# Kernel optimization log

Hardware: AMD Instinct MI355X
Metric: run time of the kernel (lower is better)

## Reference

```python
import jax, jax.numpy as jnp
import numpy as np

N_NODES = 50000
N_EDGES = 800000
IN_DIM = 128
HID = 32
HEADS = 4
OUT_DIM = 64
NEG_SLOPE = 0.2
EPS = 1e-16


def _gat_conv(x, src, dst, W, a_src, a_dst, b, heads, ch):
    """PyG GATConv (with self-loops already appended to src/dst), concat=True."""
    N = x.shape[0]
    h = (x @ W).reshape(N, heads, ch)                      # [N,H,C]
    alpha_s = jnp.einsum('nhc,hc->nh', h, a_src)           # [N,H]
    alpha_d = jnp.einsum('nhc,hc->nh', h, a_dst)           # [N,H]
    e = jax.nn.leaky_relu(alpha_s[src] + alpha_d[dst], NEG_SLOPE)  # [E,H]
    emax = jax.ops.segment_max(e, dst, num_segments=N)     # segment softmax over dst
    ex = jnp.exp(e - emax[dst])
    denom = jax.ops.segment_sum(ex, dst, num_segments=N)
    alpha = ex / (denom[dst] + EPS)                        # [E,H]
    out = jax.ops.segment_sum(h[src] * alpha[:, :, None], dst, num_segments=N)
    return out.reshape(N, heads * ch) + b


def setup_inputs() -> dict:
    key = jax.random.key(0)
    ks = jax.random.split(key, 16)
    x = jax.random.normal(ks[0], (N_NODES, IN_DIM), dtype=jnp.float32)
    edge_index = jax.random.randint(ks[1], (2, N_EDGES), 0, N_NODES, dtype=jnp.int64)

    def glorot(k, shape):
        fan = sum(shape[-2:]) if len(shape) > 1 else shape[-1]
        return jax.random.normal(k, shape, dtype=jnp.float32) * np.sqrt(2.0 / fan)

    # layer 0: IN_DIM -> HID x HEADS
    W0 = glorot(ks[2], (IN_DIM, HEADS * HID))
    as0 = glorot(ks[3], (HEADS, HID))
    ad0 = glorot(ks[4], (HEADS, HID))
    b0 = jnp.zeros((HEADS * HID,), jnp.float32)
    # layer 1: HID*HEADS -> HID x HEADS
    W1 = glorot(ks[5], (HEADS * HID, HEADS * HID))
    as1 = glorot(ks[6], (HEADS, HID))
    ad1 = glorot(ks[7], (HEADS, HID))
    b1 = jnp.zeros((HEADS * HID,), jnp.float32)
    # layer 2: HID*HEADS -> OUT_DIM, heads=1
    W2 = glorot(ks[8], (HEADS * HID, OUT_DIM))
    as2 = glorot(ks[9], (1, OUT_DIM))
    ad2 = glorot(ks[10], (1, OUT_DIM))
    b2 = jnp.zeros((OUT_DIM,), jnp.float32)
    return {"x": x, "edge_index": edge_index,
            "W0": W0, "as0": as0, "ad0": ad0, "b0": b0,
            "W1": W1, "as1": as1, "ad1": ad1, "b1": b1,
            "W2": W2, "as2": as2, "ad2": ad2, "b2": b2}


def reference(x, edge_index, W0, as0, ad0, b0, W1, as1, ad1, b1, W2, as2, ad2, b2):
    N = x.shape[0]
    # PyG GATConv default add_self_loops=True
    loops = jnp.arange(N, dtype=edge_index.dtype)
    src = jnp.concatenate([edge_index[0], loops])
    dst = jnp.concatenate([edge_index[1], loops])
    h = _gat_conv(x, src, dst, W0, as0, ad0, b0, HEADS, HID)
    h = _gat_conv(h, src, dst, W1, as1, ad1, b1, HEADS, HID)
    h = _gat_conv(h, src, dst, W2, as2, ad2, b2, 1, OUT_DIM)
    return h
```

## Files before the change

### kernel.cpp

```cpp
#include <hip/hip_runtime.h>
#include <hip/hip_fp16.h>
#include <cstdint>
#include <cstddef>

#define NEG_SLOPE 0.2f
#define EPS_F 1e-16f
#define NBLKB 64

static __device__ __forceinline__ float leaky(float x) { return x > 0.f ? x : NEG_SLOPE * x; }


__global__ __launch_bounds__(1024) void scan_k(const int* __restrict__ cnt, int* __restrict__ off, int N) {
    __shared__ int wsum[16];
    int tid = threadIdx.x;
    int lane = tid & 63, wid = tid >> 6;
    int running = 0;
    for (int base = 0; base < N; base += 1024) {
        int i = base + tid;
        int v = (i < N) ? cnt[i] : 0;
        int iv = v;
        #pragma unroll
        for (int d = 1; d < 64; d <<= 1) {
            int t = __shfl_up(iv, d);
            if (lane >= d) iv += t;
        }
        if (lane == 63) wsum[wid] = iv;
        __syncthreads();
        if (tid < 16) {
            int s = wsum[tid];
            #pragma unroll
            for (int d = 1; d < 16; d <<= 1) {
                int t = __shfl_up(s, d);
                if (tid >= d) s += t;
            }
            wsum[tid] = s;
        }
        __syncthreads();
        int add = wid ? wsum[wid - 1] : 0;
        if (i < N) off[i + 1] = running + add + iv;
        int ct = wsum[15];
        __syncthreads();
        running += ct;
    }
    if (tid == 0) off[0] = 0;
}


__global__ __launch_bounds__(256) void partB_k(const int* __restrict__ src, const int* __restrict__ dst,
                                               const int* __restrict__ starts, int* __restrict__ packed,
                                               int E, int nbuk) {
    __shared__ int lcnt[256];
    __shared__ int lbase[256];
    const int blk = blockIdx.x;
    for (int i = threadIdx.x; i < nbuk; i += 256) { lcnt[i] = 0; lbase[i] = starts[i * NBLKB + blk]; }
    __syncthreads();
    const int chunk = (E + NBLKB - 1) / NBLKB;
    const int base = blk * chunk, end = min(base + chunk, E);
    for (int i = base + (int)threadIdx.x; i < end; i += 256) {
        int d = dst[i], s = src[i];
        int b = d >> 8;
        int slot = atomicAdd(&lcnt[b], 1);
        packed[lbase[b] + slot] = s | ((d & 255) << 16);
    }
}

__global__ __launch_bounds__(256) void partC_k(const int* __restrict__ packed, const int* __restrict__ starts,
                                               int* __restrict__ off, int* __restrict__ esrc,
                                               int N, int E, int nbuk) {
    __shared__ int lcnt[256];
    __shared__ int lpre[256];
    const int b = blockIdx.x;
    const int bstart = starts[b * NBLKB];
    const int bend = (b + 1 < nbuk) ? starts[(b + 1) * NBLKB] : E;
    const int tid = threadIdx.x;
    lcnt[tid] = 0;
    __syncthreads();
    for (int i = bstart + tid; i < bend; i += 256) atomicAdd(&lcnt[packed[i] >> 16], 1);
    __syncthreads();
    if (tid < 64) {
        int v0 = lcnt[tid * 4], v1 = lcnt[tid * 4 + 1], v2 = lcnt[tid * 4 + 2], v3 = lcnt[tid * 4 + 3];
        int s = v0 + v1 + v2 + v3;
        int inc = s;
        #pragma unroll
        for (int d = 1; d < 64; d <<= 1) {
            int t = __shfl_up(inc, d);
            if (tid >= d) inc += t;
        }
        int ex = inc - s;
        lpre[tid * 4] = ex;
        lpre[tid * 4 + 1] = ex + v0;
        lpre[tid * 4 + 2] = ex + v0 + v1;
        lpre[tid * 4 + 3] = ex + v0 + v1 + v2;
    }
    __syncthreads();
    const int n0 = b << 8;
    const int nn = min(256, N - n0);
    if (tid < nn) off[n0 + tid] = bstart + lpre[tid];
    if (b == 0 && tid == 0) off[N] = E;
    lcnt[tid] = 0;
    __syncthreads();
    for (int i = bstart + tid; i < bend; i += 256) {
        int p = packed[i];
        int ld = p >> 16;
        int slot = atomicAdd(&lcnt[ld], 1);
        esrc[bstart + lpre[ld] + slot] = p & 0xFFFF;
    }
}


template <int M, int H, typename XT>
__device__ __forceinline__ void gemm_body(float* xsT, float* wt,
                                          const XT* __restrict__ X, const float* __restrict__ W,
                                          const float* __restrict__ a_s, const float* __restrict__ a_d,
                                          __half* __restrict__ O, float* __restrict__ aS,
                                          float* __restrict__ aD, int N, int bid) {
    constexpr int K = 128, BK = 16, ROWS = 128;
    constexpr int CPT = 8;
    constexpr int CT = M / CPT;
    constexpr int RPT = ROWS / (256 / CT);
    constexpr int XP = ROWS + 4;
    constexpr int C = M / H;
    constexpr int REDW = C / CPT;

    const int tid = threadIdx.x;
    const int cc = tid % CT;
    const int rr = tid / CT;
    const int row0 = bid * ROWS;

    float acc[RPT][CPT];
    #pragma unroll
    for (int r = 0; r < RPT; ++r)
        #pragma unroll
        for (int j = 0; j < CPT; ++j) acc[r][j] = 0.f;

    for (int k0 = 0; k0 < K; k0 += BK) {
        #pragma unroll
        for (int t = tid; t < ROWS * (BK / 4); t += 256) {
            int r = t >> 2;
            int kk = t & 3;
            int row = row0 + r;
            float4 v = make_float4(0.f, 0.f, 0.f, 0.f);
            if (row < N) {
                if constexpr (sizeof(XT) == 2) {
                    uint2 raw = *reinterpret_cast<const uint2*>(&X[(size_t)row * K + k0 + kk * 4]);
                    float2 fa = __half22float2(*reinterpret_cast<__half2*>(&raw.x));
                    float2 fb = __half22float2(*reinterpret_cast<__half2*>(&raw.y));
                    v = make_float4(fa.x, fa.y, fb.x, fb.y);
                } else {
                    v = *reinterpret_cast<const float4*>(&X[(size_t)row * K + k0 + kk * 4]);
                }
            }
            xsT[(kk * 4 + 0) * XP + r] = v.x;
            xsT[(kk * 4 + 1) * XP + r] = v.y;
            xsT[(kk * 4 + 2) * XP + r] = v.z;
            xsT[(kk * 4 + 3) * XP + r] = v.w;
        }
        #pragma unroll
        for (int t = tid; t < BK * (M / 4); t += 256) {
            int c4 = t % (M / 4);
            int k = t / (M / 4);
            *reinterpret_cast<float4*>(&wt[k * M + c4 * 4]) =
                *reinterpret_cast<const float4*>(&W[(size_t)(k0 + k) * M + c4 * 4]);
        }
        __syncthreads();
        #pragma unroll
        for (int k = 0; k < BK; ++k) {
            float xr[RPT];
            #pragma unroll
            for (int r4 = 0; r4 < RPT; r4 += 4) {
                float4 xv = *reinterpret_cast<const float4*>(&xsT[k * XP + rr * RPT + r4]);
                xr[r4 + 0] = xv.x; xr[r4 + 1] = xv.y; xr[r4 + 2] = xv.z; xr[r4 + 3] = xv.w;
            }
            float wv[CPT];
            #pragma unroll
            for (int c4 = 0; c4 < CPT; c4 += 4) {
                float4 w4 = *reinterpret_cast<const float4*>(&wt[k * M + cc * CPT + c4]);
                wv[c4 + 0] = w4.x; wv[c4 + 1] = w4.y; wv[c4 + 2] = w4.z; wv[c4 + 3] = w4.w;
            }
            #pragma unroll
            for (int r = 0; r < RPT; ++r)
                #pragma unroll
                for (int j = 0; j < CPT; ++j)
                    acc[r][j] = fmaf(xr[r], wv[j], acc[r][j]);
        }
        __syncthreads();
    }

    float asr[CPT], adr[CPT];
    #pragma unroll
    for (int c4 = 0; c4 < CPT; c4 += 4) {
        float4 t1 = *reinterpret_cast<const float4*>(a_s + cc * CPT + c4);
        asr[c4 + 0] = t1.x; asr[c4 + 1] = t1.y; asr[c4 + 2] = t1.z; asr[c4 + 3] = t1.w;
        float4 t2 = *reinterpret_cast<const float4*>(a_d + cc * CPT + c4);
        adr[c4 + 0] = t2.x; adr[c4 + 1] = t2.y; adr[c4 + 2] = t2.z; adr[c4 + 3] = t2.w;
    }
    const int head = (cc * CPT) / C;

    #pragma unroll
    for (int r = 0; r < RPT; ++r) {
        int row = row0 + rr * RPT + r;
        float ps = 0.f, pd = 0.f;
        #pragma unroll
        for (int j = 0; j < CPT; ++j) {
            ps = fmaf(acc[r][j], asr[j], ps);
            pd = fmaf(acc[r][j], adr[j], pd);
        }
        #pragma unroll
        for (int d = 1; d < REDW; d <<= 1) {
            ps += __shfl_xor(ps, d);
            pd += __shfl_xor(pd, d);
        }
        if (row < N) {
            __half2 p0 = __float22half2_rn(make_float2(acc[r][0], acc[r][1]));
            __half2 p1 = __float22half2_rn(make_float2(acc[r][2], acc[r][3]));
            __half2 p2 = __float22half2_rn(make_float2(acc[r][4], acc[r][5]));
            __half2 p3 = __float22half2_rn(make_float2(acc[r][6], acc[r][7]));
            uint4 pk;
            pk.x = *reinterpret_cast<unsigned*>(&p0);
            pk.y = *reinterpret_cast<unsigned*>(&p1);
            pk.z = *reinterpret_cast<unsigned*>(&p2);
            pk.w = *reinterpret_cast<unsigned*>(&p3);
            *reinterpret_cast<uint4*>(&O[(size_t)row * M + cc * CPT]) = pk;
            if ((cc & (REDW - 1)) == 0) {
                aS[(size_t)row * H + head] = ps;
                aD[(size_t)row * H + head] = pd;
            }
        }
    }
}

template <int M, int H, typename XT>
__global__ __launch_bounds__(256, 2) void gemm_k(const XT* __restrict__ X, const float* __restrict__ W,
                                                 const float* __restrict__ a_s, const float* __restrict__ a_d,
                                                 __half* __restrict__ O, float* __restrict__ aS,
                                                 float* __restrict__ aD, int N) {
    __shared__ float smem[16 * 132 + 16 * M];
    gemm_body<M, H, XT>(smem, smem + 16 * 132, X, W, a_s, a_d, O, aS, aD, N, blockIdx.x);
}

template <int M, int H>
__global__ __launch_bounds__(256, 2) void gemm_hist_k(const float* __restrict__ X, const float* __restrict__ W,
                                                      const float* __restrict__ a_s, const float* __restrict__ a_d,
                                                      __half* __restrict__ O, float* __restrict__ aS,
                                                      float* __restrict__ aD, int N,
                                                      const int* __restrict__ dst, int E,
                                                      int* __restrict__ cnts, int gemmGrid, int nbuk) {
    __shared__ float smem[16 * 132 + 16 * M];
    if ((int)blockIdx.x < gemmGrid) {
        gemm_body<M, H, float>(smem, smem + 16 * 132, X, W, a_s, a_d, O, aS, aD, N, blockIdx.x);
    } else {
        int* lcnt = (int*)smem;
        const int blk = blockIdx.x - gemmGrid;
        for (int i = threadIdx.x; i < nbuk; i += 256) lcnt[i] = 0;
        __syncthreads();
        const int chunk = (E + NBLKB - 1) / NBLKB;
        const int base = blk * chunk, end = min(base + chunk, E);
        for (int i = base + (int)threadIdx.x; i < end; i += 256) atomicAdd(&lcnt[dst[i] >> 8], 1);
        __syncthreads();
        for (int b = threadIdx.x; b < nbuk; b += 256) cnts[b * NBLKB + blk] = lcnt[b];
    }
}


template <int H, int C, typename OutT>
__global__ __launch_bounds__(256) void agg_k(const __half* __restrict__ h, const float* __restrict__ aS,
                                             const float* __restrict__ aD, const int* __restrict__ off,
                                             const int* __restrict__ esrc, const float* __restrict__ bias,
                                             OutT* __restrict__ out, int N) {
    constexpr int M = H * C;
    constexpr int CPL = M / 32;
    __shared__ float wlds[4][2][32][H];
    const int wslot = threadIdx.x >> 6;
    const int lane  = threadIdx.x & 63;
    const int g     = lane >> 5;
    const int lg    = lane & 31;
    const int node  = (blockIdx.x * 4 + wslot) * 2 + g;
    const bool valid = node < N;
    const int nd = valid ? node : N - 1;

    float adv[H], asv[H];
    if constexpr (H == 4) {
        float4 t = *reinterpret_cast<const float4*>(aD + (size_t)nd * 4);
        adv[0] = t.x; adv[1] = t.y; adv[2] = t.z; adv[3] = t.w;
        float4 u = *reinterpret_cast<const float4*>(aS + (size_t)nd * 4);
        asv[0] = u.x; asv[1] = u.y; asv[2] = u.z; asv[3] = u.w;
    } else {
        adv[0] = aD[nd]; asv[0] = aS[nd];
    }
    float eself[H];
    #pragma unroll
    for (int q = 0; q < H; ++q) eself[q] = leaky(asv[q] + adv[q]);

    const int s0 = off[nd], s1 = off[nd + 1];
    const int deg = s1 - s0;

    if (__all(deg < 32)) {
        const int sv = (lg < deg) ? esrc[s0 + lg] : nd;
        const int ch0 = lg * CPL;
        const int hd = ch0 / C;
        const int cnt = deg + 1;
        const int cmax = max(cnt, __shfl_xor(cnt, 32));
        float wsum = 0.f;

        if constexpr (CPL == 4) {
            uint2 A[8], B[8];
            #pragma unroll
            for (int t = 0; t < 8; ++t) {
                int s = __shfl(sv, t, 32);
                A[t] = *reinterpret_cast<const uint2*>(h + (size_t)s * M + ch0);
            }
            if (cmax > 8) {
                #pragma unroll
                for (int t = 0; t < 8; ++t) {
                    int s = __shfl(sv, 8 + t, 32);
                    B[t] = *reinterpret_cast<const uint2*>(h + (size_t)s * M + ch0);
                }
            }
            {
                float4 u = *reinterpret_cast<const float4*>(aS + (size_t)sv * 4);
                float4 wv;
                if (lg < deg) {
                    wv.x = __expf(leaky(u.x + adv[0]));
                    wv.y = __expf(leaky(u.y + adv[1]));
                    wv.z = __expf(leaky(u.z + adv[2]));
                    wv.w = __expf(leaky(u.w + adv[3]));
                } else if (lg == deg) {
                    wv = make_float4(__expf(eself[0]), __expf(eself[1]), __expf(eself[2]), __expf(eself[3]));
                } else {
                    wv = make_float4(0.f, 0.f, 0.f, 0.f);
                }
                *reinterpret_cast<float4*>(&wlds[wslot][g][lg][0]) = wv;
            }
            asm volatile("s_waitcnt lgkmcnt(0)" ::: "memory");

            float acc0 = 0.f, acc1 = 0.f, acc2 = 0.f, acc3 = 0.f;
            auto refill = [&](uint2 (&buf)[8], int j) {
                #pragma unroll
                for (int t = 0; t < 8; ++t) {
                    int s = __shfl(sv, j + t, 32);
                    buf[t] = *reinterpret_cast<const uint2*>(h + (size_t)s * M + ch0);
                }
            };
            auto consume = [&](uint2 (&buf)[8], int j) {
                #pragma unroll
                for (int t = 0; t < 8; ++t) {
                    float wq = wlds[wslot][g][j + t][hd];
                    wsum += wq;
                    float2 fa = __half22float2(*reinterpret_cast<__half2*>(&buf[t].x));
                    float2 fb = __half22float2(*reinterpret_cast<__half2*>(&buf[t].y));
                    acc0 = fmaf(wq, fa.x, acc0);
                    acc1 = fmaf(wq, fa.y, acc1);
                    acc2 = fmaf(wq, fb.x, acc2);
                    acc3 = fmaf(wq, fb.y, acc3);
                }
            };
            consume(A, 0);
            if (cmax > 8) {
                if (cmax > 16) refill(A, 16);
                consume(B, 8);
                if (cmax > 16) {
                    if (cmax > 24) refill(B, 24);
                    consume(A, 16);
                    if (cmax > 24) consume(B, 24);
                }
            }
            if (valid) {
                float inv = 1.f / (wsum + EPS_F);
                float4 bb = *reinterpret_cast<const float4*>(bias + ch0);
                float o0 = acc0 * inv + bb.x, o1 = acc1 * inv + bb.y;
                float o2 = acc2 * inv + bb.z, o3 = acc3 * inv + bb.w;
                if constexpr (sizeof(OutT) == 4) {
                    *reinterpret_cast<float4*>((float*)out + (size_t)nd * M + ch0) = make_float4(o0, o1, o2, o3);
                } else {
                    __half2 q0 = __float22half2_rn(make_float2(o0, o1));
                    __half2 q1 = __float22half2_rn(make_float2(o2, o3));
                    uint2 pk;
                    pk.x = *reinterpret_cast<unsigned*>(&q0);
                    pk.y = *reinterpret_cast<unsigned*>(&q1);
                    *reinterpret_cast<uint2*>((__half*)out + (size_t)nd * M + ch0) = pk;
                }
            }
        } else {
            unsigned A[8], B[8];
            #pragma unroll
            for (int t = 0; t < 8; ++t) {
                int s = __shfl(sv, t, 32);
                A[t] = *reinterpret_cast<const unsigned*>(h + (size_t)s * M + ch0);
            }
            if (cmax > 8) {
                #pragma unroll
                for (int t = 0; t < 8; ++t) {
                    int s = __shfl(sv, 8 + t, 32);
                    B[t] = *reinterpret_cast<const unsigned*>(h + (size_t)s * M + ch0);
                }
            }
            {
                float u = aS[sv];
                wlds[wslot][g][lg][0] = (lg < deg) ? __expf(leaky(u + adv[0]))
                                      : (lg == deg) ? __expf(eself[0]) : 0.f;
            }
            asm volatile("s_waitcnt lgkmcnt(0)" ::: "memory");

            float acc0 = 0.f, acc1 = 0.f;
            auto refill = [&](unsigned (&buf)[8], int j) {
                #pragma unroll
                for (int t = 0; t < 8; ++t) {
                    int s = __shfl(sv, j + t, 32);
                    buf[t] = *reinterpret_cast<const unsigned*>(h + (size_t)s * M + ch0);
                }
            };
            auto consume = [&](unsigned (&buf)[8], int j) {
                #pragma unroll
                for (int t = 0; t < 8; ++t) {
                    float wq = wlds[wslot][g][j + t][0];
                    wsum += wq;
                    float2 fa = __half22float2(*reinterpret_cast<__half2*>(&buf[t]));
                    acc0 = fmaf(wq, fa.x, acc0);
                    acc1 = fmaf(wq, fa.y, acc1);
                }
            };
            consume(A, 0);
            if (cmax > 8) {
                if (cmax > 16) refill(A, 16);
                consume(B, 8);
                if (cmax > 16) {
                    if (cmax > 24) refill(B, 24);
                    consume(A, 16);
                    if (cmax > 24) consume(B, 24);
                }
            }
            if (valid) {
                float inv = 1.f / (wsum + EPS_F);
                float o0 = acc0 * inv + bias[ch0];
                float o1 = acc1 * inv + bias[ch0 + 1];
                if constexpr (sizeof(OutT) == 4) {
                    *reinterpret_cast<float2*>((float*)out + (size_t)nd * M + ch0) = make_float2(o0, o1);
                } else {
                    __half2 q0 = __float22half2_rn(make_float2(o0, o1));
                    *reinterpret_cast<unsigned*>((__half*)out + (size_t)nd * M + ch0) =
                        *reinterpret_cast<unsigned*>(&q0);
                }
            }
        }
    } else {
        constexpr int CPL64 = M / 64;
        const int ch = lane * CPL64;
        const int hh = ch / C;
        #pragma unroll 1
        for (int i = 0; i < 2; ++i) {
            int fn = (blockIdx.x * 4 + wslot) * 2 + i;
            if (fn >= N) continue;
            float fadv[H], fes[H];
            if constexpr (H == 4) {
                float4 t = *reinterpret_cast<const float4*>(aD + (size_t)fn * 4);
                fadv[0] = t.x; fadv[1] = t.y; fadv[2] = t.z; fadv[3] = t.w;
                float4 u = *reinterpret_cast<const float4*>(aS + (size_t)fn * 4);
                fes[0] = leaky(u.x + t.x); fes[1] = leaky(u.y + t.y);
                fes[2] = leaky(u.z + t.z); fes[3] = leaky(u.w + t.w);
            } else {
                fadv[0] = aD[fn];
                fes[0] = leaky(aS[fn] + fadv[0]);
            }
            int fs0 = off[fn], fs1 = off[fn + 1];
            float m[H], ds[H];
            #pragma unroll
            for (int q = 0; q < H; ++q) { m[q] = fes[q]; ds[q] = 0.f; }
            for (int e = fs0 + lane; e < fs1; e += 64) {
                int s = esrc[e];
                if constexpr (H == 4) {
                    float4 u = *reinterpret_cast<const float4*>(aS + (size_t)s * 4);
                    float evv[4] = {u.x, u.y, u.z, u.w};
                    #pragma unroll
                    for (int q = 0; q < 4; ++q) {
                        float ee = leaky(evv[q] + fadv[q]);
                        float nm = fmaxf(m[q], ee);
                        ds[q] = ds[q] * __expf(m[q] - nm) + __expf(ee - nm);
                        m[q] = nm;
                    }
                } else {
                    float ee = leaky(aS[s] + fadv[0]);
                    float nm = fmaxf(m[0], ee);
                    ds[0] = ds[0] * __expf(m[0] - nm) + __expf(ee - nm);
                    m[0] = nm;
                }
            }
            #pragma unroll
            for (int q = 0; q < H; ++q) {
                #pragma unroll
                for (int d = 1; d < 64; d <<= 1) {
                    float om = __shfl_xor(m[q], d);
                    float od = __shfl_xor(ds[q], d);
                    float nm = fmaxf(m[q], om);
                    ds[q] = ds[q] * __expf(m[q] - nm) + od * __expf(om - nm);
                    m[q] = nm;
                }
                ds[q] += __expf(fes[q] - m[q]);
            }
            float a0 = 0.f, a1 = 0.f;
            for (int e = fs0; e < fs1; ++e) {
                int s = esrc[e];
                float wq = __expf(leaky(aS[(size_t)s * H + hh] + fadv[hh]) - m[hh]);
                if constexpr (CPL64 == 2) {
                    float2 f = __half22float2(*reinterpret_cast<const __half2*>(h + (size_t)s * M + ch));
                    a0 = fmaf(wq, f.x, a0);
                    a1 = fmaf(wq, f.y, a1);
                } else {
                    a0 = fmaf(wq, __half2float(h[(size_t)s * M + ch]), a0);
                }
            }
            {
                float wq = __expf(fes[hh] - m[hh]);
                if constexpr (CPL64 == 2) {
                    float2 f = __half22float2(*reinterpret_cast<const __half2*>(h + (size_t)fn * M + ch));
                    a0 = fmaf(wq, f.x, a0);
                    a1 = fmaf(wq, f.y, a1);
                } else {
                    a0 = fmaf(wq, __half2float(h[(size_t)fn * M + ch]), a0);
                }
            }
            float inv = 1.f / (ds[hh] + EPS_F);
            if constexpr (CPL64 == 2) {
                float o0 = a0 * inv + bias[ch], o1 = a1 * inv + bias[ch + 1];
                if constexpr (sizeof(OutT) == 4) {
                    *reinterpret_cast<float2*>((float*)out + (size_t)fn * M + ch) = make_float2(o0, o1);
                } else {
                    __half2 q0 = __float22half2_rn(make_float2(o0, o1));
                    *reinterpret_cast<unsigned*>((__half*)out + (size_t)fn * M + ch) =
                        *reinterpret_cast<unsigned*>(&q0);
                }
            } else {
                float o0 = a0 * inv + bias[ch];
                if constexpr (sizeof(OutT) == 4) ((float*)out)[(size_t)fn * M + ch] = o0;
                else ((__half*)out)[(size_t)fn * M + ch] = __float2half_rn(o0);
            }
        }
    }
}


extern "C" void kernel_launch(void* const* d_in, const int* in_sizes, int n_in,
                              void* d_out, int out_size, void* d_ws, size_t ws_size,
                              hipStream_t stream) {
    const float* x   = (const float*)d_in[0];
    const int*   ei  = (const int*)d_in[1];
    const float* W0  = (const float*)d_in[2];
    const float* as0 = (const float*)d_in[3];
    const float* ad0 = (const float*)d_in[4];
    const float* b0  = (const float*)d_in[5];
    const float* W1  = (const float*)d_in[6];
    const float* as1 = (const float*)d_in[7];
    const float* ad1 = (const float*)d_in[8];
    const float* b1  = (const float*)d_in[9];
    const float* W2  = (const float*)d_in[10];
    const float* as2 = (const float*)d_in[11];
    const float* ad2 = (const float*)d_in[12];
    const float* b2  = (const float*)d_in[13];

    const int N = in_sizes[0] / 128;
    const int E = in_sizes[1] / 2;
    const int* esrc_in = ei;
    const int* edst_in = ei + E;
    const int NBUK = (N + 255) >> 8;

    char* w = (char*)d_ws;
    auto carve = [&](size_t bytes) -> char* {
        char* p = w;
        w += (bytes + 255) & ~(size_t)255;
        return p;
    };
    int*    off    = (int*)carve((size_t)(N + 1) * 4);
    int*    es     = (int*)carve((size_t)E * 4);
    int*    cnts   = (int*)carve((size_t)NBUK * NBLKB * 4);
    int*    starts = (int*)carve(((size_t)NBUK * NBLKB + 1) * 4);
    int*    packed = (int*)carve((size_t)E * 4);
    float*  aS     = (float*)carve((size_t)N * 4 * sizeof(float));
    float*  aD     = (float*)carve((size_t)N * 4 * sizeof(float));
    __half* bufH   = (__half*)carve((size_t)N * 128 * sizeof(__half));
    __half* bufO   = (__half*)carve((size_t)N * 128 * sizeof(__half));
    (void)ws_size; (void)n_in; (void)out_size;

    const int GEMM_GRID = (N + 127) / 128;
    const int AGG_GRID = (N + 7) / 8;

    gemm_hist_k<128, 4><<<GEMM_GRID + NBLKB, 256, 0, stream>>>(x, W0, as0, ad0, bufH, aS, aD, N,
                                                               edst_in, E, cnts, GEMM_GRID, NBUK);
    scan_k<<<1, 1024, 0, stream>>>(cnts, starts, NBUK * NBLKB);
    partB_k<<<NBLKB, 256, 0, stream>>>(esrc_in, edst_in, starts, packed, E, NBUK);
    partC_k<<<NBUK, 256, 0, stream>>>(packed, starts, off, es, N, E, NBUK);

    agg_k<4, 32, __half><<<AGG_GRID, 256, 0, stream>>>(bufH, aS, aD, off, es, b0, bufO, N);

    gemm_k<128, 4, __half><<<GEMM_GRID, 256, 0, stream>>>(bufO, W1, as1, ad1, bufH, aS, aD, N);
    agg_k<4, 32, __half><<<AGG_GRID, 256, 0, stream>>>(bufH, aS, aD, off, es, b1, bufO, N);

    gemm_k<64, 1, __half><<<GEMM_GRID, 256, 0, stream>>>(bufO, W2, as2, ad2, bufH, aS, aD, N);
    agg_k<1, 64, float><<<AGG_GRID, 256, 0, stream>>>(bufH, aS, aD, off, es, b2, (float*)d_out, N);
}
```

Measured before the change: 250.9 us.

## Enlarge aggregation blocks to 1024 threads and prefetch third neighbor batch

Result: slower. 263.3 us (+4.9%).

```diff
diff --git a/kernel.cpp b/kernel.cpp
--- a/kernel.cpp
+++ b/kernel.cpp
@@ -263,18 +263,18 @@
 
 
 template <int H, int C, typename OutT>
-__global__ __launch_bounds__(256) void agg_k(const __half* __restrict__ h, const float* __restrict__ aS,
-                                             const float* __restrict__ aD, const int* __restrict__ off,
-                                             const int* __restrict__ esrc, const float* __restrict__ bias,
-                                             OutT* __restrict__ out, int N) {
+__global__ __launch_bounds__(1024) void agg_k(const __half* __restrict__ h, const float* __restrict__ aS,
+                                              const float* __restrict__ aD, const int* __restrict__ off,
+                                              const int* __restrict__ esrc, const float* __restrict__ bias,
+                                              OutT* __restrict__ out, int N) {
     constexpr int M = H * C;
     constexpr int CPL = M / 32;
-    __shared__ float wlds[4][2][32][H];
+    __shared__ float wlds[16][2][32][H];
     const int wslot = threadIdx.x >> 6;
     const int lane  = threadIdx.x & 63;
     const int g     = lane >> 5;
     const int lg    = lane & 31;
-    const int node  = (blockIdx.x * 4 + wslot) * 2 + g;
+    const int node  = (blockIdx.x * 16 + wslot) * 2 + g;
     const bool valid = node < N;
     const int nd = valid ? node : N - 1;
 
@@ -303,7 +303,7 @@
         float wsum = 0.f;
 
         if constexpr (CPL == 4) {
-            uint2 A[8], B[8];
+            uint2 A[8], B[8], Cb[8];
             #pragma unroll
             for (int t = 0; t < 8; ++t) {
                 int s = __shfl(sv, t, 32);
@@ -314,6 +314,13 @@
                 for (int t = 0; t < 8; ++t) {
                     int s = __shfl(sv, 8 + t, 32);
                     B[t] = *reinterpret_cast<const uint2*>(h + (size_t)s * M + ch0);
+                }
+            }
+            if (cmax > 16) {
+                #pragma unroll
+                for (int t = 0; t < 8; ++t) {
+                    int s = __shfl(sv, 16 + t, 32);
+                    Cb[t] = *reinterpret_cast<const uint2*>(h + (size_t)s * M + ch0);
                 }
             }
             {
@@ -334,13 +341,6 @@
             asm volatile("s_waitcnt lgkmcnt(0)" ::: "memory");
 
             float acc0 = 0.f, acc1 = 0.f, acc2 = 0.f, acc3 = 0.f;
-            auto refill = [&](uint2 (&buf)[8], int j) {
-                #pragma unroll
-                for (int t = 0; t < 8; ++t) {
-                    int s = __shfl(sv, j + t, 32);
-                    buf[t] = *reinterpret_cast<const uint2*>(h + (size_t)s * M + ch0);
-                }
-            };
             auto consume = [&](uint2 (&buf)[8], int j) {
                 #pragma unroll
                 for (int t = 0; t < 8; ++t) {
@@ -356,12 +356,17 @@
             };
             consume(A, 0);
             if (cmax > 8) {
-                if (cmax > 16) refill(A, 16);
+                if (cmax > 24) {
+                    #pragma unroll
+                    for (int t = 0; t < 8; ++t) {
+                        int s = __shfl(sv, 24 + t, 32);
+                        A[t] = *reinterpret_cast<const uint2*>(h + (size_t)s * M + ch0);
+                    }
+                }
                 consume(B, 8);
                 if (cmax > 16) {
-                    if (cmax > 24) refill(B, 24);
-                    consume(A, 16);
-                    if (cmax > 24) consume(B, 24);
+                    consume(Cb, 16);
+                    if (cmax > 24) consume(A, 24);
                 }
             }
             if (valid) {
@@ -381,7 +386,7 @@
                 }
             }
         } else {
-            unsigned A[8], B[8];
+            unsigned A[8], B[8], Cb[8];
             #pragma unroll
             for (int t = 0; t < 8; ++t) {
                 int s = __shfl(sv, t, 32);
@@ -392,6 +397,13 @@
                 for (int t = 0; t < 8; ++t) {
                     int s = __shfl(sv, 8 + t, 32);
                     B[t] = *reinterpret_cast<const unsigned*>(h + (size_t)s * M + ch0);
+                }
+            }
+            if (cmax > 16) {
+                #pragma unroll
+                for (int t = 0; t < 8; ++t) {
+                    int s = __shfl(sv, 16 + t, 32);
+                    Cb[t] = *reinterpret_cast<const unsigned*>(h + (size_t)s * M + ch0);
                 }
             }
             {
@@ -402,13 +414,6 @@
             asm volatile("s_waitcnt lgkmcnt(0)" ::: "memory");
 
             float acc0 = 0.f, acc1 = 0.f;
-            auto refill = [&](unsigned (&buf)[8], int j) {
-                #pragma unroll
-                for (int t = 0; t < 8; ++t) {
-                    int s = __shfl(sv, j + t, 32);
-                    buf[t] = *reinterpret_cast<const unsigned*>(h + (size_t)s * M + ch0);
-                }
-            };
             auto consume = [&](unsigned (&buf)[8], int j) {
                 #pragma unroll
                 for (int t = 0; t < 8; ++t) {
@@ -421,12 +426,17 @@
             };
             consume(A, 0);
             if (cmax > 8) {
-                if (cmax > 16) refill(A, 16);
+                if (cmax > 24) {
+                    #pragma unroll
+                    for (int t = 0; t < 8; ++t) {
+                        int s = __shfl(sv, 24 + t, 32);
+                        A[t] = *reinterpret_cast<const unsigned*>(h + (size_t)s * M + ch0);
+                    }
+                }
                 consume(B, 8);
                 if (cmax > 16) {
-                    if (cmax > 24) refill(B, 24);
-                    consume(A, 16);
-                    if (cmax > 24) consume(B, 24);
+                    consume(Cb, 16);
+                    if (cmax > 24) consume(A, 24);
                 }
             }
             if (valid) {
@@ -448,7 +458,7 @@
         const int hh = ch / C;
         #pragma unroll 1
         for (int i = 0; i < 2; ++i) {
-            int fn = (blockIdx.x * 4 + wslot) * 2 + i;
+            int fn = (blockIdx.x * 16 + wslot) * 2 + i;
             if (fn >= N) continue;
             float fadv[H], fes[H];
             if constexpr (H == 4) {
@@ -580,7 +590,7 @@
     (void)ws_size; (void)n_in; (void)out_size;
 
     const int GEMM_GRID = (N + 127) / 128;
-    const int AGG_GRID = (N + 7) / 8;
+    const int AGG_GRID = (N + 31) / 32;
 
     gemm_hist_k<128, 4><<<GEMM_GRID + NBLKB, 256, 0, stream>>>(x, W0, as0, ad0, bufH, aS, aD, N,
                                                                edst_in, E, cnts, GEMM_GRID, NBUK);
@@ -588,11 +598,11 @@
     partB_k<<<NBLKB, 256, 0, stream>>>(esrc_in, edst_in, starts, packed, E, NBUK);
     partC_k<<<NBUK, 256, 0, stream>>>(packed, starts, off, es, N, E, NBUK);
 
-    agg_k<4, 32, __half><<<AGG_GRID, 256, 0, stream>>>(bufH, aS, aD, off, es, b0, bufO, N);
+    agg_k<4, 32, __half><<<AGG_GRID, 1024, 0, stream>>>(bufH, aS, aD, off, es, b0, bufO, N);
 
     gemm_k<128, 4, __half><<<GEMM_GRID, 256, 0, stream>>>(bufO, W1, as1, ad1, bufH, aS, aD, N);
-    agg_k<4, 32, __half><<<AGG_GRID, 256, 0, stream>>>(bufH, aS, aD, off, es, b1, bufO, N);
+    agg_k<4, 32, __half><<<AGG_GRID, 1024, 0, stream>>>(bufH, aS, aD, off, es, b1, bufO, N);
 
     gemm_k<64, 1, __half><<<GEMM_GRID, 256, 0, stream>>>(bufO, W2, as2, ad2, bufH, aS, aD, N);
-    agg_k<1, 64, float><<<AGG_GRID, 256, 0, stream>>>(bufH, aS, aD, off, es, b2, (float*)d_out, N);
-}
+    agg_k<1, 64, float><<<AGG_GRID, 1024, 0, stream>>>(bufH, aS, aD, off, es, b2, (float*)d_out, N);
+}
```
